# Performance work log

Hardware: AMD Instinct MI355X
Metric: run time of the kernel (lower is better)

The kernel has to match this reference:

```python
import jax, jax.numpy as jnp
import numpy as np

DEPTH = 12
N_FEATURES = 512
BATCH = 16384
N_NODES = 2 ** DEPTH - 1   # 4095 internal nodes, concatenated level-by-level
N_LEAVES = 2 ** DEPTH      # 4096


def setup_inputs() -> dict:
    key = jax.random.key(0)
    k_x, k_w, k_b, k_s, k_l = jax.random.split(key, 5)
    x_input = jax.random.normal(k_x, (BATCH, N_FEATURES), dtype=jnp.float32)
    # Per-level Linear(n_features, 2**d) weights concatenated on the output dim:
    # level d occupies rows [2**d - 1, 2**(d+1) - 1).
    bound = 1.0 / np.sqrt(N_FEATURES)  # torch Linear default init scale
    W_all = jax.random.uniform(k_w, (N_NODES, N_FEATURES), dtype=jnp.float32,
                               minval=-bound, maxval=bound)
    b_all = jax.random.uniform(k_b, (N_NODES,), dtype=jnp.float32,
                               minval=-bound, maxval=bound)
    # original uses max(randn, 1) -> positive steepness >= 1
    s_all = jax.random.uniform(k_s, (N_NODES,), dtype=jnp.float32,
                               minval=1.0, maxval=2.0)
    leaves = jax.random.normal(k_l, (N_LEAVES,), dtype=jnp.float32)
    return {"x_input": x_input, "W_all": W_all, "b_all": b_all,
            "s_all": s_all, "leaves": leaves}


def reference(x_input, W_all, b_all, s_all, leaves):
    B = x_input.shape[0]
    # One fused GEMM for all depth levels: [B, 2**depth - 1]
    logits = x_input @ W_all.T + b_all
    p_all = jax.nn.sigmoid(logits * s_all)
    # Recursive path-probability product down the binary tree.
    # out[:, j] at level d is the prob of reaching child j (j = 2*node + side),
    # matching the original dict insertion order (node ascending, left then right).
    out = jnp.ones((B, 1), dtype=p_all.dtype)
    for d in range(DEPTH):
        start = 2 ** d - 1
        p = p_all[:, start:start + 2 ** d]          # [B, 2**d]
        # interleave left (parent*p) and right (parent*(1-p)) children
        out = jnp.stack([out * p, out * (1.0 - p)], axis=-1).reshape(B, 2 ** (d + 1))
    # weighted sum over leaves
    return (jax.nn.sigmoid(leaves) * out).sum(axis=1)   # [B]
```

## Files before the change

kernel.cpp:

```cpp
#include <hip/hip_runtime.h>
#include <hip/hip_bf16.h>

#define M_DIM   16384
#define K_DIM   512
#define NNODES  4095
#define NPERM   4096
#define NTOP    128
#define NWROWS  (NPERM + NTOP)
#define NBOT_BLOCKS (32 * 128)
#define NTOT_BLOCKS (NBOT_BLOCKS + 128)

typedef __bf16   bf16x8 __attribute__((ext_vector_type(8)));
typedef float    floatx4 __attribute__((ext_vector_type(4)));

__device__ __forceinline__ float sigmoidf_(float z) {
    return __builtin_amdgcn_rcpf(1.f + __expf(-z));
}

__device__ __forceinline__ void gld_lds16(const void* g, void* l) {
    __builtin_amdgcn_global_load_lds(
        (const __attribute__((address_space(1))) void*)g,
        (__attribute__((address_space(3))) void*)l, 16, 0, 0);
}

__global__ __launch_bounds__(256) void cvt_all(const float* __restrict__ X,
                                               const float* __restrict__ W,
                                               const float* __restrict__ bias,
                                               const float* __restrict__ scale,
                                               __hip_bfloat16* __restrict__ Xb,
                                               __hip_bfloat16* __restrict__ Wb,
                                               float* __restrict__ bp,
                                               float* __restrict__ sp) {
    const int bid = blockIdx.x;
    if (bid < 4096) {
        const int idx = (bid * 256 + threadIdx.x) * 8;
        float4 f0 = *reinterpret_cast<const float4*>(X + idx);
        float4 f1 = *reinterpret_cast<const float4*>(X + idx + 4);
        __hip_bfloat16 h[8];
        h[0] = __float2bfloat16(f0.x); h[1] = __float2bfloat16(f0.y);
        h[2] = __float2bfloat16(f0.z); h[3] = __float2bfloat16(f0.w);
        h[4] = __float2bfloat16(f1.x); h[5] = __float2bfloat16(f1.y);
        h[6] = __float2bfloat16(f1.z); h[7] = __float2bfloat16(f1.w);
        *reinterpret_cast<int4*>(Xb + idx) = *reinterpret_cast<int4*>(h);
        return;
    }
    const int idx = ((bid - 4096) * 256 + threadIdx.x) * 8;
    const int r = idx >> 9;
    const int k = idx & 511;
    int node;
    if (r < NPERM) {
        const int t = r >> 5, o = r & 31;
        int d, q;
        if (o < 16)       { d = 11; q = o; }
        else if (o < 24)  { d = 10; q = o - 16; }
        else if (o < 28)  { d = 9;  q = o - 24; }
        else if (o < 30)  { d = 8;  q = o - 28; }
        else if (o == 30) { d = 7;  q = 0; }
        else              { d = -1; q = 0; }
        node = (d < 0) ? -1 : ((1 << d) - 1 + (t << (d - 7)) + q);
    } else {
        const int c = r - NPERM;
        node = (c < 127) ? c : -1;
    }
    __hip_bfloat16 h[8];
    if (node >= 0) {
        const float* src = W + (size_t)node * 512 + k;
        float4 f0 = *reinterpret_cast<const float4*>(src);
        float4 f1 = *reinterpret_cast<const float4*>(src + 4);
        h[0] = __float2bfloat16(f0.x); h[1] = __float2bfloat16(f0.y);
        h[2] = __float2bfloat16(f0.z); h[3] = __float2bfloat16(f0.w);
        h[4] = __float2bfloat16(f1.x); h[5] = __float2bfloat16(f1.y);
        h[6] = __float2bfloat16(f1.z); h[7] = __float2bfloat16(f1.w);
    } else {
        #pragma unroll
        for (int i = 0; i < 8; ++i) h[i] = __float2bfloat16(0.f);
    }
    *reinterpret_cast<int4*>(Wb + idx) = *reinterpret_cast<int4*>(h);
    if (k == 0) {
        bp[r] = (node >= 0) ? bias[node]  : 0.f;
        sp[r] = (node >= 0) ? scale[node] : 1.f;
    }
}

#define PT_STRIDE 135
__global__ __launch_bounds__(256) void gemm_fold(
    const __hip_bfloat16* __restrict__ A,
    const __hip_bfloat16* __restrict__ B,
    const float* __restrict__ bp,
    const float* __restrict__ sp,
    const float* __restrict__ leaves,
    float* __restrict__ partial,
    _Float16* __restrict__ ptop)
{
    __shared__ char smem[35072] __attribute__((aligned(16)));
    __hip_bfloat16* lA = (__hip_bfloat16*)smem;
    __hip_bfloat16* lB = lA + 8192;
    _Float16* pt  = (_Float16*)smem;
    float*    slf = (float*)(smem + 34560);

    const int tid  = threadIdx.x;
    const int lane = tid & 63;
    const int wv   = tid >> 6;
    const int bid  = blockIdx.x;
    int tile_m, tile_n;
    if (bid < NBOT_BLOCKS) { tile_m = bid >> 5; tile_n = bid & 31; }
    else                   { tile_m = bid - NBOT_BLOCKS; tile_n = 32; }
    const int m0 = tile_m * 128;
    const int n0 = tile_n * 128;

    if (tile_n < 32 && tid < 128) slf[tid] = sigmoidf_(leaves[n0 + tid]);

    const int wm = (wv >> 1) * 64;
    const int wn = (wv & 1) * 64;
    const int lrow = lane >> 3;
    const int swzb = ((lane & 7) ^ lrow) * 16;
    const int quad = lane >> 4;
    const int l15  = lane & 15;
    const int xr   = l15 & 7;

    floatx4 acc[4][4];
    #pragma unroll
    for (int i = 0; i < 4; ++i)
        #pragma unroll
        for (int j = 0; j < 4; ++j)
            acc[i][j] = (floatx4){0.f, 0.f, 0.f, 0.f};

    for (int k0 = 0; k0 < K_DIM; k0 += 64) {
        #pragma unroll
        for (int i = 0; i < 4; ++i) {
            const int rbase = i * 32 + wv * 8;
            const char* gA = (const char*)(A + (size_t)(m0 + rbase + lrow) * K_DIM + k0) + swzb;
            const char* gB = (const char*)(B + (size_t)(n0 + rbase + lrow) * K_DIM + k0) + swzb;
            gld_lds16(gA, &lA[rbase * 64]);
            gld_lds16(gB, &lB[rbase * 64]);
        }
        __syncthreads();
        #pragma unroll
        for (int kk = 0; kk < 64; kk += 32) {
            const int cb = ((kk >> 3) + quad) ^ xr;
            bf16x8 af[4], bfr[4];
            #pragma unroll
            for (int i = 0; i < 4; ++i)
                af[i] = *reinterpret_cast<const bf16x8*>(
                    &lA[(wm + i * 16 + l15) * 64 + cb * 8]);
            #pragma unroll
            for (int j = 0; j < 4; ++j)
                bfr[j] = *reinterpret_cast<const bf16x8*>(
                    &lB[(wn + j * 16 + l15) * 64 + cb * 8]);
            #pragma unroll
            for (int i = 0; i < 4; ++i)
                #pragma unroll
                for (int j = 0; j < 4; ++j)
                    acc[i][j] = __builtin_amdgcn_mfma_f32_16x16x32_bf16(
                        af[i], bfr[j], acc[i][j], 0, 0, 0);
        }
        __syncthreads();
    }

    float bn[4], sn[4];
    #pragma unroll
    for (int j = 0; j < 4; ++j) {
        const int n = n0 + wn + j * 16 + l15;
        bn[j] = bp[n];
        sn[j] = sp[n];
    }

    if (tile_n == 32) {
        #pragma unroll
        for (int i = 0; i < 4; ++i) {
            #pragma unroll
            for (int r = 0; r < 4; ++r) {
                const int m = m0 + wm + i * 16 + quad * 4 + r;
                #pragma unroll
                for (int j = 0; j < 4; ++j) {
                    const int col = wn + j * 16 + l15;
                    ptop[(size_t)m * 128 + col] =
                        (_Float16)sigmoidf_((acc[i][j][r] + bn[j]) * sn[j]);
                }
            }
        }
        return;
    }

    #pragma unroll
    for (int i = 0; i < 4; ++i) {
        #pragma unroll
        for (int r = 0; r < 4; ++r) {
            const int row = wm + i * 16 + quad * 4 + r;
            #pragma unroll
            for (int j = 0; j < 4; ++j) {
                const int col = wn + j * 16 + l15;
                pt[row * PT_STRIDE + col] =
                    (_Float16)sigmoidf_((acc[i][j][r] + bn[j]) * sn[j]);
            }
        }
    }
    __syncthreads();

    #pragma unroll
    for (int z = 0; z < 2; ++z) {
        const int task = tid + z * 256;
        const int row  = task >> 2;
        const int t    = task & 3;
        const _Float16* pp = pt + row * PT_STRIDE + t * 32;
        const float*    sl = slf + t * 32;
        float v[16];
        #pragma unroll
        for (int q = 0; q < 16; ++q) {
            const float p = (float)pp[q];
            v[q] = p * sl[2 * q] + (1.f - p) * sl[2 * q + 1];
        }
        #pragma unroll
        for (int q = 0; q < 8; ++q) {
            const float p = (float)pp[16 + q];
            v[q] = p * v[2 * q] + (1.f - p) * v[2 * q + 1];
        }
        #pragma unroll
        for (int q = 0; q < 4; ++q) {
            const float p = (float)pp[24 + q];
            v[q] = p * v[2 * q] + (1.f - p) * v[2 * q + 1];
        }
        #pragma unroll
        for (int q = 0; q < 2; ++q) {
            const float p = (float)pp[28 + q];
            v[q] = p * v[2 * q] + (1.f - p) * v[2 * q + 1];
        }
        const float p7 = (float)pp[30];
        partial[(size_t)(m0 + row) * 128 + tile_n * 4 + t] =
            p7 * v[0] + (1.f - p7) * v[1];
    }
}

__global__ __launch_bounds__(256) void final_fold(
    const float* __restrict__ partial,
    const _Float16* __restrict__ ptop,
    float* __restrict__ out)
{
    __shared__ float    pL[64 * 129];
    __shared__ _Float16 pq[64 * 134];

    const int tid = threadIdx.x;
    const int m0  = blockIdx.x * 64;

    #pragma unroll
    for (int it = 0; it < 32; ++it) {
        const int idx = tid + it * 256;
        const int row = idx >> 7;
        const int c   = idx & 127;
        pL[row * 129 + c] = partial[(size_t)(m0 + row) * 128 + c];
        pq[row * 134 + c] = ptop[(size_t)(m0 + row) * 128 + c];
    }
    __syncthreads();

    if (tid < 64) {
        float* v = pL + tid * 129;
        const _Float16* pr = pq + tid * 134;
        #pragma unroll
        for (int d = 6; d >= 1; --d) {
            const int base = (1 << d) - 1;
            const int cnt  = 1 << d;
            for (int q = 0; q < cnt; ++q) {
                const float p = (float)pr[base + q];
                v[q] = p * v[2 * q] + (1.f - p) * v[2 * q + 1];
            }
        }
        const float p0 = (float)pr[0];
        out[m0 + tid] = p0 * v[0] + (1.f - p0) * v[1];
    }
}

__global__ __launch_bounds__(256) void tnn_fallback(
    const float* __restrict__ X, const float* __restrict__ W,
    const float* __restrict__ bias, const float* __restrict__ scale,
    const float* __restrict__ leaves, float* __restrict__ out)
{
    __shared__ float xr[512];
    __shared__ float sl[4096];
    __shared__ float pp[4096];
    __shared__ float v0[2048];
    __shared__ float v1[1024];
    const int tid  = threadIdx.x;
    const int lane = tid & 63;
    const int wv   = tid >> 6;
    const int b    = blockIdx.x;
    for (int i = tid; i < 512;  i += 256) xr[i] = X[(size_t)b * 512 + i];
    for (int i = tid; i < 4096; i += 256) sl[i] = sigmoidf_(leaves[i]);
    __syncthreads();
    for (int n = wv; n < NNODES; n += 4) {
        float sum = 0.f;
        const float* wr = W + (size_t)n * 512;
        for (int k = lane; k < 512; k += 64) sum += xr[k] * wr[k];
        #pragma unroll
        for (int off = 32; off; off >>= 1) sum += __shfl_xor(sum, off);
        if (lane == 0) pp[n] = sigmoidf_((sum + bias[n]) * scale[n]);
    }
    __syncthreads();
    for (int j = tid; j < 2048; j += 256) {
        const float p = pp[2047 + j];
        v0[j] = p * sl[2 * j] + (1.f - p) * sl[2 * j + 1];
    }
    __syncthreads();
    float* src = v0;
    float* dst = v1;
    for (int d = 10; d >= 0; --d) {
        const int width = 1 << d;
        const int start = width - 1;
        for (int j = tid; j < width; j += 256) {
            const float p = pp[start + j];
            dst[j] = p * src[2 * j] + (1.f - p) * src[2 * j + 1];
        }
        __syncthreads();
        float* t = src; src = dst; dst = t;
    }
    if (tid == 0) out[b] = src[0];
}

extern "C" void kernel_launch(void* const* d_in, const int* in_sizes, int n_in,
                              void* d_out, int out_size, void* d_ws, size_t ws_size,
                              hipStream_t stream) {
    const float* X      = (const float*)d_in[0];
    const float* W      = (const float*)d_in[1];
    const float* bias   = (const float*)d_in[2];
    const float* scale  = (const float*)d_in[3];
    const float* leaves = (const float*)d_in[4];
    float* out = (float*)d_out;

    const size_t offX  = 0;
    const size_t offW  = (size_t)M_DIM * K_DIM * 2;
    const size_t offB  = offW + (size_t)NWROWS * K_DIM * 2;
    const size_t offS  = offB + (size_t)NWROWS * 4;
    const size_t offP  = offS + (size_t)NWROWS * 4;
    const size_t offT  = offP + (size_t)M_DIM * 128 * 4;
    const size_t need  = offT + (size_t)M_DIM * 128 * 2;

    if (ws_size >= need) {
        __hip_bfloat16* Xb = (__hip_bfloat16*)((char*)d_ws + offX);
        __hip_bfloat16* Wb = (__hip_bfloat16*)((char*)d_ws + offW);
        float* bp = (float*)((char*)d_ws + offB);
        float* sp = (float*)((char*)d_ws + offS);
        float* partial = (float*)((char*)d_ws + offP);
        _Float16* ptop = (_Float16*)((char*)d_ws + offT);
        cvt_all<<<4096 + 1056, 256, 0, stream>>>(X, W, bias, scale, Xb, Wb, bp, sp);
        gemm_fold<<<NTOT_BLOCKS, 256, 0, stream>>>(
            Xb, Wb, bp, sp, leaves, partial, ptop);
        final_fold<<<M_DIM / 64, 256, 0, stream>>>(partial, ptop, out);
    } else {
        tnn_fallback<<<M_DIM, 256, 0, stream>>>(X, W, bias, scale, leaves, out);
    }
}
```

Measured before the change: 217.7 us.

## Double-buffer LDS tiles with K-step of 32 and prefetch next slice

The GEMM main loop moves from a single 64-wide K tile to two 32-wide LDS buffers, using a matching XOR swizzle. The next K slice is issued with global_load_lds before the MFMAs run on the current buffer. This is meant to overlap global-to-LDS traffic with matrix math and to halve the barriers per K step from two to one. The cost is twice as many loop iterations, each carrying fewer MFMAs, plus a possible wait on the loads at every barrier.

After: 196.3 us. 9.8% less time.

```diff
diff --git a/kernel.cpp b/kernel.cpp
--- a/kernel.cpp
+++ b/kernel.cpp
@@ -83,6 +83,7 @@
 }
 
 #define PT_STRIDE 135
+#define BUFB 16384
 __global__ __launch_bounds__(256) void gemm_fold(
     const __hip_bfloat16* __restrict__ A,
     const __hip_bfloat16* __restrict__ B,
@@ -93,8 +94,6 @@
     _Float16* __restrict__ ptop)
 {
     __shared__ char smem[35072] __attribute__((aligned(16)));
-    __hip_bfloat16* lA = (__hip_bfloat16*)smem;
-    __hip_bfloat16* lB = lA + 8192;
     _Float16* pt  = (_Float16*)smem;
     float*    slf = (float*)(smem + 34560);
 
@@ -112,11 +111,25 @@
 
     const int wm = (wv >> 1) * 64;
     const int wn = (wv & 1) * 64;
-    const int lrow = lane >> 3;
-    const int swzb = ((lane & 7) ^ lrow) * 16;
     const int quad = lane >> 4;
     const int l15  = lane & 15;
-    const int xr   = l15 & 7;
+
+    const int srow = lane >> 2;
+    const int gc   = (lane & 3) ^ (srow & 3);
+    const int sgoff = srow * (K_DIM * 2) + gc * 16;
+
+    const char* gAp[2];
+    const char* gBp[2];
+    char* sA[2];
+    char* sB[2];
+    #pragma unroll
+    for (int i = 0; i < 2; ++i) {
+        const int rbase = wv * 32 + i * 16;
+        gAp[i] = (const char*)(A + (size_t)(m0 + rbase) * K_DIM) + sgoff;
+        gBp[i] = (const char*)(B + (size_t)(n0 + rbase) * K_DIM) + sgoff;
+        sA[i] = smem + rbase * 64;
+        sB[i] = smem + 8192 + rbase * 64;
+    }
 
     floatx4 acc[4][4];
     #pragma unroll
@@ -125,37 +138,47 @@
         for (int j = 0; j < 4; ++j)
             acc[i][j] = (floatx4){0.f, 0.f, 0.f, 0.f};
 
-    for (int k0 = 0; k0 < K_DIM; k0 += 64) {
-        #pragma unroll
-        for (int i = 0; i < 4; ++i) {
-            const int rbase = i * 32 + wv * 8;
-            const char* gA = (const char*)(A + (size_t)(m0 + rbase + lrow) * K_DIM + k0) + swzb;
-            const char* gB = (const char*)(B + (size_t)(n0 + rbase + lrow) * K_DIM + k0) + swzb;
-            gld_lds16(gA, &lA[rbase * 64]);
-            gld_lds16(gB, &lB[rbase * 64]);
-        }
+    #pragma unroll
+    for (int i = 0; i < 2; ++i) {
+        gld_lds16(gAp[i], sA[i]);
+        gld_lds16(gBp[i], sB[i]);
+        gAp[i] += 64; gBp[i] += 64;
+    }
+
+    const int cbr = quad ^ (l15 & 3);
+
+    #pragma unroll 1
+    for (int k0 = 0; k0 < 16; ++k0) {
         __syncthreads();
-        #pragma unroll
-        for (int kk = 0; kk < 64; kk += 32) {
-            const int cb = ((kk >> 3) + quad) ^ xr;
-            bf16x8 af[4], bfr[4];
+        if (k0 < 15) {
+            const int boff = ((k0 + 1) & 1) * BUFB;
             #pragma unroll
-            for (int i = 0; i < 4; ++i)
-                af[i] = *reinterpret_cast<const bf16x8*>(
-                    &lA[(wm + i * 16 + l15) * 64 + cb * 8]);
+            for (int i = 0; i < 2; ++i) {
+                gld_lds16(gAp[i], sA[i] + boff);
+                gld_lds16(gBp[i], sB[i] + boff);
+                gAp[i] += 64; gBp[i] += 64;
+            }
+        }
+        const __hip_bfloat16* cA =
+            (const __hip_bfloat16*)(smem + (k0 & 1) * BUFB);
+        const __hip_bfloat16* cB = cA + 4096;
+        bf16x8 af[4], bfr[4];
+        #pragma unroll
+        for (int i = 0; i < 4; ++i)
+            af[i] = *reinterpret_cast<const bf16x8*>(
+                &cA[(wm + i * 16 + l15) * 32 + cbr * 8]);
+        #pragma unroll
+        for (int j = 0; j < 4; ++j)
+            bfr[j] = *reinterpret_cast<const bf16x8*>(
+                &cB[(wn + j * 16 + l15) * 32 + cbr * 8]);
+        #pragma unroll
+        for (int i = 0; i < 4; ++i)
             #pragma unroll
             for (int j = 0; j < 4; ++j)
-                bfr[j] = *reinterpret_cast<const bf16x8*>(
-                    &lB[(wn + j * 16 + l15) * 64 + cb * 8]);
-            #pragma unroll
-            for (int i = 0; i < 4; ++i)
-                #pragma unroll
-                for (int j = 0; j < 4; ++j)
-                    acc[i][j] = __builtin_amdgcn_mfma_f32_16x16x32_bf16(
-                        af[i], bfr[j], acc[i][j], 0, 0, 0);
-        }
-        __syncthreads();
-    }
+                acc[i][j] = __builtin_amdgcn_mfma_f32_16x16x32_bf16(
+                    af[i], bfr[j], acc[i][j], 0, 0, 0);
+    }
+    __syncthreads();
 
     float bn[4], sn[4];
     #pragma unroll
```
